# Performance work log

Measured on AMD Instinct MI355X. Metric: run time of the kernel, lower is better.

Reference implementation:

```python
import jax, jax.numpy as jnp
import numpy as np

DILATION = 3
SUBSIZE = 16
TOPK = 16


def _forward(fm1, fm2):
    bs, c, h, w = fm1.shape
    d = min(h, w, DILATION)   # dilation clamp: sorted([h, w, dilation])[0]
    s = min(h, w, SUBSIZE)    # subsize clamp
    nby, nbx = h // s, w // s
    # non-overlapping sub-blocks of fm1: (bs, c, nby, nbx, s, s)
    blk = fm1.reshape(bs, c, nby, s, nbx, s).transpose(0, 1, 2, 4, 3, 5)
    ys = jnp.arange(nby) * s
    xs = jnp.arange(nbx) * s
    offs = jnp.arange(s)
    # all (dh, dw) shifts in [-d, d]^2
    dhs, dws = jnp.meshgrid(jnp.arange(-d, d + 1), jnp.arange(-d, d + 1), indexing='ij')
    shifts = jnp.stack([dhs.reshape(-1), dws.reshape(-1)], axis=-1)  # ((2d+1)^2, 2)
    denom = jnp.asarray(c * s * s, fm1.dtype)  # per-sample element count of a block

    def step(carry, shift):
        dh, dw = shift[0], shift[1]
        # boundary clamp of the fm2 window origin (matches the if/elif ladder)
        y0 = jnp.clip(ys + dh, 0, h - s)
        x0 = jnp.clip(xs + dw, 0, w - s)
        ri = y0[:, None] + offs[None, :]  # (nby, s)
        ci = x0[:, None] + offs[None, :]  # (nbx, s)
        # gathered fm2 windows: (bs, c, nby, nbx, s, s)
        win = fm2[:, :, ri[:, None, :, None], ci[None, :, None, :]]
        # per-sample MSE per block: sum over (c, s, s) / (c*s*s)
        dist = jnp.sum((blk - win) ** 2, axis=(1, 4, 5)) / denom  # (bs, nby, nbx)
        return jnp.minimum(carry, dist.reshape(bs, -1)), None

    init = jnp.full((bs, nby * nbx), jnp.inf, dtype=fm1.dtype)
    min_per_block, _ = jax.lax.scan(step, init, shifts)  # (bs, nblocks)

    nblocks = nby * nbx
    if 0 <= TOPK <= nblocks:
        # sum of the TOPK smallest block distances per sample
        smallest = -jax.lax.top_k(-min_per_block, TOPK)[0]
        return jnp.sum(smallest, axis=-1)
    return jnp.sum(min_per_block, axis=-1)


def setup_inputs() -> dict:
    key = jax.random.key(0)
    k1, k2 = jax.random.split(key)
    fm1 = jax.random.normal(k1, (8, 64, 192, 192), dtype=jnp.float32)
    fm2 = jax.random.normal(k2, (8, 64, 192, 192), dtype=jnp.float32)
    return {"fm1": fm1, "fm2": fm2}


def reference(fm1, fm2):
    return _forward(fm1, fm2)
```

## Files before the change

### kernel.cpp

```cpp
#include <hip/hip_runtime.h>
#include <math.h>

#define HH 192
#define WW 192
#define CC 64
#define CHW (HH*WW)
#define SS 16
#define NB 12
#define NBLK 144
#define CCH 8
#define UROW 22
#define LROW 28
#define QN 6
#define NSH 49
#define STAGE_N (CCH*UROW*QN)

__device__ __forceinline__ int iclamp(int v, int lo, int hi){ return v<lo?lo:(v>hi?hi:v); }

template<int EX, int OX, int NCH>
__device__ __forceinline__ void run_chunks(
    const float* __restrict__ f1b, const float* __restrict__ f2b,
    float* sm, int tid, int t, int y, int h8, bool active,
    int ys, int xs, int rbase, int ey, int cc0, float acc[7])
{
  const int cbase4 = (EX == -3) ? 0 : ((EX == 0) ? (xs - 4) : (WW - LROW + 4));
  const int oyt = iclamp(t + ey, 0, 6);
  const float* ap0 = f1b + (size_t)(ys + y)*WW + xs + h8;
  const int wrow = (y + oyt)*LROW + h8;

  for (int ch0 = 0; ch0 < NCH; ch0 += CCH) {
    const int cc = cc0 + ch0;
    for (int i = tid; i < STAGE_N; i += 256) {
      int ch  = i / (UROW*QN);
      int rem = i - ch*(UROW*QN);
      int r   = rem / QN;
      int q   = rem - r*QN;
      *(float4*)&sm[ch*(UROW*LROW) + r*LROW + 4*q] =
        *(const float4*)(f2b + (size_t)(cc+ch)*CHW + (size_t)(rbase+r)*WW + cbase4 + 4*q);
    }
    __syncthreads();

    if (active) {
#pragma unroll 2
      for (int c = 0; c < CCH; c++) {
        const float* ap = ap0 + (size_t)(cc + c)*CHW;
        float a[8];
        {
          float4 v0 = *(const float4*)(ap + 0);
          float4 v1 = *(const float4*)(ap + 4);
          a[0]=v0.x; a[1]=v0.y; a[2]=v0.z; a[3]=v0.w;
          a[4]=v1.x; a[5]=v1.y; a[6]=v1.z; a[7]=v1.w;
        }
        const float* wp = sm + c*(UROW*LROW) + wrow;
        float w[16];
#pragma unroll
        for (int j = 0; j < 4; j++) {
          float4 v = *(const float4*)(wp + 4*j);
          w[4*j]=v.x; w[4*j+1]=v.y; w[4*j+2]=v.z; w[4*j+3]=v.w;
        }
#pragma unroll
        for (int u = 0; u < 7; u++) {
          const int o = ((u+EX) < 0 ? 0 : ((u+EX) > 6 ? 6 : (u+EX))) + OX;
          float s0 = 0.f, s1 = 0.f;
#pragma unroll
          for (int x = 0; x < 8; x += 2) {
            float d0 = a[x]   - w[o+x];
            float d1 = a[x+1] - w[o+x+1];
            s0 = fmaf(d0, d0, s0);
            s1 = fmaf(d1, d1, s1);
          }
          acc[u] += s0 + s1;
        }
      }
    }
    __syncthreads();
  }
}

template<int NZ>
__global__ __launch_bounds__(256, 8) void dist_kernel(
    const float* __restrict__ fm1, const float* __restrict__ fm2,
    float* __restrict__ partial)
{
  __shared__ float sm[CCH*UROW*LROW];

  const int wg  = blockIdx.x;
  const int z   = wg >= 8*NBLK ? 1 : 0;
  const int w2  = wg - z*8*NBLK;
  const int b   = w2 & 7;
  const int blk = w2 >> 3;
  const int by  = blk / NB, bx = blk - by*NB;
  const int ys  = by*SS, xs = bx*SS;
  const int rbase = iclamp(ys-3, 0, HH-UROW);
  const int ey = (ys-3) - rbase;

  const int tid = threadIdx.x;
  const int t   = tid >> 5;
  const int y   = (tid & 31) >> 1;
  const int h8  = (tid & 1) * 8;
  const bool active = (t < 7);

  const float* f1b = fm1 + (size_t)b*CC*CHW;
  const float* f2b = fm2 + (size_t)b*CC*CHW;

  const int cc0 = z * (CC/NZ);

  float acc[7];
#pragma unroll
  for (int k = 0; k < 7; k++) acc[k] = 0.f;

  if (bx == 0)
    run_chunks<-3,0,CC/NZ>(f1b, f2b, sm, tid, t, y, h8, active, ys, xs, rbase, ey, cc0, acc);
  else if (bx == NB-1)
    run_chunks< 3,2,CC/NZ>(f1b, f2b, sm, tid, t, y, h8, active, ys, xs, rbase, ey, cc0, acc);
  else
    run_chunks< 0,1,CC/NZ>(f1b, f2b, sm, tid, t, y, h8, active, ys, xs, rbase, ey, cc0, acc);

  float* distk = sm;
#pragma unroll
  for (int u = 0; u < 7; u++) {
    float v = acc[u];
#pragma unroll
    for (int off = 16; off; off >>= 1) v += __shfl_xor(v, off);
    if (active && (tid & 31) == 0) distk[t*7 + u] = v;
  }
  __syncthreads();

  if constexpr (NZ == 2) {
    if (tid < NSH)
      partial[((size_t)(b*NBLK + blk)*NZ + z)*NSH + tid] = distk[tid];
  } else {
    if (tid < 64) {
      float v = (tid < NSH) ? distk[tid] : __builtin_inff();
#pragma unroll
      for (int off = 32; off; off >>= 1) v = fminf(v, __shfl_xor(v, off));
      if (tid == 0) partial[(size_t)b*NBLK + blk] = v;
    }
  }
}

template<int NZ>
__global__ void topk_kernel(const float* __restrict__ partial, float* __restrict__ out)
{
  const int b = blockIdx.x;
  const int lane = threadIdx.x;
  const float INF = __builtin_inff();

  float v0 = INF, v1 = INF, v2 = INF;
  if constexpr (NZ == 2) {
#pragma unroll
    for (int i = 0; i < 3; i++) {
      int blk = lane + 64*i;
      if (blk < NBLK) {
        const float* p = partial + (size_t)(b*NBLK + blk)*2*NSH;
        float m = INF;
        for (int k = 0; k < NSH; k++) m = fminf(m, p[k] + p[k+NSH]);
        if (i == 0) v0 = m; else if (i == 1) v1 = m; else v2 = m;
      }
    }
  } else {
    const float* p = partial + (size_t)b*NBLK;
    v0 = p[lane];
    v1 = p[lane + 64];
    v2 = (lane < 16) ? p[lane + 128] : INF;
  }

  float sum = 0.f;
  for (int it = 0; it < 16; ++it) {
    float lm = fminf(v0, fminf(v1, v2));
    float m = lm;
#pragma unroll
    for (int off = 32; off; off >>= 1) m = fminf(m, __shfl_xor(m, off));
    sum += m;
    unsigned long long mask = __ballot(lm == m);
    int leader = __ffsll(mask) - 1;
    if (lane == leader) {
      if (v0 == m)      v0 = INF;
      else if (v1 == m) v1 = INF;
      else              v2 = INF;
    }
  }
  if (lane == 0) out[b] = sum * (1.0f/((float)CC*SS*SS));
}

extern "C" void kernel_launch(void* const* d_in, const int* in_sizes, int n_in,
                              void* d_out, int out_size, void* d_ws, size_t ws_size,
                              hipStream_t stream)
{
  const float* fm1 = (const float*)d_in[0];
  const float* fm2 = (const float*)d_in[1];
  float* out  = (float*)d_out;
  float* scratch = (float*)d_ws;

  const size_t NEED = (size_t)8 * NBLK * 2 * NSH * sizeof(float);
  if (ws_size >= NEED) {
    dist_kernel<2><<<2*8*NBLK, 256, 0, stream>>>(fm1, fm2, scratch);
    topk_kernel<2><<<8, 64, 0, stream>>>(scratch, out);
  } else {
    dist_kernel<1><<<8*NBLK, 256, 0, stream>>>(fm1, fm2, scratch);
    topk_kernel<1><<<8, 64, 0, stream>>>(scratch, out);
  }
}
```

Before: 95.66 us.

## Expand squared distance into norms minus cross-correlation, using idle warp for window norms

Rewrites the per-shift block distance as ||a||^2 - 2<a,w> + ||w||^2. This turns the inner loop from a subtract plus FMA into a single FMA per element. The previously idle eighth warp now computes per-row window squared norms with a sliding sum, and warp 0 accumulates the fm1 block norm. Shared-memory rows also get a small per-row offset, meant to reduce LDS bank conflicts. The trade-off is fp32 cancellation risk from the expanded form, plus extra combine work at the end.

```diff
diff --git a/kernel.cpp b/kernel.cpp
--- a/kernel.cpp
+++ b/kernel.cpp
@@ -14,33 +14,41 @@
 #define QN 6
 #define NSH 49
 #define STAGE_N (CCH*UROW*QN)
+#define CORR0 0
+#define WACC0 (CORR0 + NSH)
+#define ASUM0 (WACC0 + UROW*7)
 
 __device__ __forceinline__ int iclamp(int v, int lo, int hi){ return v<lo?lo:(v>hi?hi:v); }
+__device__ __forceinline__ int rowoff(int r){ return ((r>>3)&1)*4; }
 
 template<int EX, int OX, int NCH>
 __device__ __forceinline__ void run_chunks(
     const float* __restrict__ f1b, const float* __restrict__ f2b,
-    float* sm, int tid, int t, int y, int h8, bool active,
-    int ys, int xs, int rbase, int ey, int cc0, float acc[7])
+    float* sm, int tid, int t, int y, int h8,
+    int ys, int xs, int rbase, int ey, int cc0,
+    float acc[7], float wacc[7], float& asum)
 {
   const int cbase4 = (EX == -3) ? 0 : ((EX == 0) ? (xs - 4) : (WW - LROW + 4));
   const int oyt = iclamp(t + ey, 0, 6);
   const float* ap0 = f1b + (size_t)(ys + y)*WW + xs + h8;
-  const int wrow = (y + oyt)*LROW + h8;
+  const int wrow = (y + oyt)*LROW + rowoff(y + oyt) + h8;
+  const bool isCorr = (t < 7);
+  const int r = tid - 224;
+  const bool isWrow = (t == 7) && (r < UROW);
 
   for (int ch0 = 0; ch0 < NCH; ch0 += CCH) {
     const int cc = cc0 + ch0;
     for (int i = tid; i < STAGE_N; i += 256) {
       int ch  = i / (UROW*QN);
       int rem = i - ch*(UROW*QN);
-      int r   = rem / QN;
-      int q   = rem - r*QN;
-      *(float4*)&sm[ch*(UROW*LROW) + r*LROW + 4*q] =
-        *(const float4*)(f2b + (size_t)(cc+ch)*CHW + (size_t)(rbase+r)*WW + cbase4 + 4*q);
+      int rr  = rem / QN;
+      int q   = rem - rr*QN;
+      *(float4*)&sm[ch*(UROW*LROW) + rr*LROW + rowoff(rr) + 4*q] =
+        *(const float4*)(f2b + (size_t)(cc+ch)*CHW + (size_t)(rbase+rr)*WW + cbase4 + 4*q);
     }
     __syncthreads();
 
-    if (active) {
+    if (isCorr) {
 #pragma unroll 2
       for (int c = 0; c < CCH; c++) {
         const float* ap = ap0 + (size_t)(cc + c)*CHW;
@@ -51,6 +59,10 @@
           a[0]=v0.x; a[1]=v0.y; a[2]=v0.z; a[3]=v0.w;
           a[4]=v1.x; a[5]=v1.y; a[6]=v1.z; a[7]=v1.w;
         }
+        if (t == 0) {
+          asum = fmaf(a[0],a[0], fmaf(a[1],a[1], fmaf(a[2],a[2], fmaf(a[3],a[3], asum))));
+          asum = fmaf(a[4],a[4], fmaf(a[5],a[5], fmaf(a[6],a[6], fmaf(a[7],a[7], asum))));
+        }
         const float* wp = sm + c*(UROW*LROW) + wrow;
         float w[16];
 #pragma unroll
@@ -64,12 +76,31 @@
           float s0 = 0.f, s1 = 0.f;
 #pragma unroll
           for (int x = 0; x < 8; x += 2) {
-            float d0 = a[x]   - w[o+x];
-            float d1 = a[x+1] - w[o+x+1];
-            s0 = fmaf(d0, d0, s0);
-            s1 = fmaf(d1, d1, s1);
+            s0 = fmaf(a[x],   w[o+x],   s0);
+            s1 = fmaf(a[x+1], w[o+x+1], s1);
           }
           acc[u] += s0 + s1;
+        }
+      }
+    } else if (isWrow) {
+      const int rbOff = r*LROW + rowoff(r);
+#pragma unroll 1
+      for (int c = 0; c < CCH; c++) {
+        const float* wp = sm + c*(UROW*LROW) + rbOff;
+        float w[24];
+#pragma unroll
+        for (int j = 0; j < 6; j++) {
+          float4 v = *(const float4*)(wp + 4*j);
+          w[4*j]=v.x; w[4*j+1]=v.y; w[4*j+2]=v.z; w[4*j+3]=v.w;
+        }
+        float W = 0.f;
+#pragma unroll
+        for (int x = 0; x < 16; x++) W = fmaf(w[OX+x], w[OX+x], W);
+        wacc[0] += W;
+#pragma unroll
+        for (int oo = 1; oo < 7; oo++) {
+          W += w[OX+oo+15]*w[OX+oo+15] - w[OX+oo-1]*w[OX+oo-1];
+          wacc[oo] += W;
         }
       }
     }
@@ -85,7 +116,7 @@
   __shared__ float sm[CCH*UROW*LROW];
 
   const int wg  = blockIdx.x;
-  const int z   = wg >= 8*NBLK ? 1 : 0;
+  const int z   = (NZ == 2 && wg >= 8*NBLK) ? 1 : 0;
   const int w2  = wg - z*8*NBLK;
   const int b   = w2 & 7;
   const int blk = w2 >> 3;
@@ -93,48 +124,74 @@
   const int ys  = by*SS, xs = bx*SS;
   const int rbase = iclamp(ys-3, 0, HH-UROW);
   const int ey = (ys-3) - rbase;
+  const int cbase = iclamp(xs-3, 0, WW-UROW);
+  const int ex = (xs-3) - cbase;
 
   const int tid = threadIdx.x;
   const int t   = tid >> 5;
   const int y   = (tid & 31) >> 1;
   const int h8  = (tid & 1) * 8;
-  const bool active = (t < 7);
 
   const float* f1b = fm1 + (size_t)b*CC*CHW;
   const float* f2b = fm2 + (size_t)b*CC*CHW;
-
   const int cc0 = z * (CC/NZ);
 
-  float acc[7];
-#pragma unroll
-  for (int k = 0; k < 7; k++) acc[k] = 0.f;
+  float acc[7], wacc[7];
+#pragma unroll
+  for (int k = 0; k < 7; k++) { acc[k] = 0.f; wacc[k] = 0.f; }
+  float asum = 0.f;
 
   if (bx == 0)
-    run_chunks<-3,0,CC/NZ>(f1b, f2b, sm, tid, t, y, h8, active, ys, xs, rbase, ey, cc0, acc);
+    run_chunks<-3,0,CC/NZ>(f1b, f2b, sm, tid, t, y, h8, ys, xs, rbase, ey, cc0, acc, wacc, asum);
   else if (bx == NB-1)
-    run_chunks< 3,2,CC/NZ>(f1b, f2b, sm, tid, t, y, h8, active, ys, xs, rbase, ey, cc0, acc);
+    run_chunks< 3,2,CC/NZ>(f1b, f2b, sm, tid, t, y, h8, ys, xs, rbase, ey, cc0, acc, wacc, asum);
   else
-    run_chunks< 0,1,CC/NZ>(f1b, f2b, sm, tid, t, y, h8, active, ys, xs, rbase, ey, cc0, acc);
-
-  float* distk = sm;
+    run_chunks< 0,1,CC/NZ>(f1b, f2b, sm, tid, t, y, h8, ys, xs, rbase, ey, cc0, acc, wacc, asum);
+
 #pragma unroll
   for (int u = 0; u < 7; u++) {
     float v = acc[u];
 #pragma unroll
     for (int off = 16; off; off >>= 1) v += __shfl_xor(v, off);
-    if (active && (tid & 31) == 0) distk[t*7 + u] = v;
+    if (t < 7 && (tid & 31) == 0) sm[CORR0 + t*7 + u] = v;
+  }
+  {
+    const int r = tid - 224;
+    if (t == 7 && r < UROW) {
+#pragma unroll
+      for (int oo = 0; oo < 7; oo++) sm[WACC0 + r*7 + oo] = wacc[oo];
+    }
+  }
+  {
+    float v = asum;
+#pragma unroll
+    for (int off = 16; off; off >>= 1) v += __shfl_xor(v, off);
+    if (tid == 0) sm[ASUM0] = v;
   }
   __syncthreads();
 
   if constexpr (NZ == 2) {
-    if (tid < NSH)
-      partial[((size_t)(b*NBLK + blk)*NZ + z)*NSH + tid] = distk[tid];
+    if (tid < NSH) {
+      int tt = tid / 7, u = tid - 7*tt;
+      int oyt = iclamp(tt + ey, 0, 6);
+      int oi  = iclamp(u + ex, 0, 6);
+      float s = sm[ASUM0] - 2.f*sm[CORR0 + tid];
+#pragma unroll
+      for (int yy = 0; yy < 16; ++yy) s += sm[WACC0 + (yy + oyt)*7 + oi];
+      partial[((size_t)(b*NBLK + blk)*2 + z)*NSH + tid] = s;
+    }
   } else {
     if (tid < 64) {
-      float v = (tid < NSH) ? distk[tid] : __builtin_inff();
-#pragma unroll
-      for (int off = 32; off; off >>= 1) v = fminf(v, __shfl_xor(v, off));
-      if (tid == 0) partial[(size_t)b*NBLK + blk] = v;
+      int tu = tid < NSH ? tid : NSH-1;
+      int tt = tu / 7, u = tu - 7*tt;
+      int oyt = iclamp(tt + ey, 0, 6);
+      int oi  = iclamp(u + ex, 0, 6);
+      float s = sm[ASUM0] - 2.f*sm[CORR0 + tu];
+#pragma unroll
+      for (int yy = 0; yy < 16; ++yy) s += sm[WACC0 + (yy + oyt)*7 + oi];
+#pragma unroll
+      for (int off = 32; off; off >>= 1) s = fminf(s, __shfl_xor(s, off));
+      if (tid == 0) partial[(size_t)b*NBLK + blk] = s;
     }
   }
 }
```

Measured after the change: 112.0 us. 17.1% more time.
